# Kernel optimization log

Hardware: AMD Instinct MI355X
Metric: run time of the kernel (lower is better)

The kernel has to match this reference:

```python
import jax, jax.numpy as jnp
import numpy as np

C_PARAM = 2.0
EPS = 1e-05

def setup_inputs() -> dict:
    key = jax.random.key(0)
    x = jax.random.normal(key, (2048, 512, 7, 7), dtype=jnp.float32)
    return {"x": x}

def reference(x) -> jnp.ndarray:
    # y[n,c] = spatial mean over HW
    y = jnp.mean(x, axis=(2, 3))                      # [N, C]
    # per-sample channel stats (biased variance, matching mean(x^2)-mean^2)
    m = jnp.mean(y, axis=1, keepdims=True)            # [N, 1]
    mx2 = jnp.mean(y * y, axis=1, keepdims=True)      # [N, 1]
    var = jnp.maximum(mx2 - m * m, 0.0)
    inv_std = jax.lax.rsqrt(var + EPS)
    y_norm = (y - m) * inv_std                        # [N, C]
    gate = jnp.exp(-0.5 * C_PARAM * y_norm * y_norm)  # [N, C]
    return x * gate[:, :, None, None]
```

## Files before the change

kernel.cpp:

```cpp
#include <hip/hip_runtime.h>
#include <math.h>


#define NN 2048
#define CC 512
#define HW 49
#define CHCH 128
#define CHEL (CHCH * HW)
#define CHV4 (CHEL / 4)
#define NCHUNK (CC / CHCH)
#define EPS 1e-5f

__global__ __launch_bounds__(512) void stats_kernel(const float* __restrict__ x,
                                                    float* __restrict__ gate) {
    __shared__ float lds[CHEL];
    __shared__ float wsum[8];
    __shared__ float wsum2[8];
    __shared__ float s_m, s_inv;

    const int n = blockIdx.x;
    const int tid = threadIdx.x;
    const size_t nbase = (size_t)n * (CC * HW);
    const float4* __restrict__ xin4 = (const float4*)(x + nbase);

    float y = 0.0f;
    for (int j = 0; j < NCHUNK; ++j) {
        for (int i = tid; i < CHV4; i += 512) {
            ((float4*)lds)[i] = xin4[j * CHV4 + i];
        }
        __syncthreads();
        if ((tid >> 7) == j) {
            const int base = (tid & (CHCH - 1)) * HW;
            float s = 0.0f;
#pragma unroll
            for (int l = 0; l < HW; ++l) s += lds[base + l];
            y = s * (1.0f / (float)HW);
        }
        __syncthreads();
    }

    float sum = y, sum2 = y * y;
#pragma unroll
    for (int off = 32; off > 0; off >>= 1) {
        sum  += __shfl_down(sum, off);
        sum2 += __shfl_down(sum2, off);
    }
    const int wave = tid >> 6;
    const int lane = tid & 63;
    if (lane == 0) { wsum[wave] = sum; wsum2[wave] = sum2; }
    __syncthreads();
    if (tid == 0) {
        float ts = 0.0f, ts2 = 0.0f;
#pragma unroll
        for (int w = 0; w < 8; ++w) { ts += wsum[w]; ts2 += wsum2[w]; }
        const float m = ts * (1.0f / (float)CC);
        float var = ts2 * (1.0f / (float)CC) - m * m;
        var = fmaxf(var, 0.0f);
        s_m = m;
        s_inv = rsqrtf(var + EPS);
    }
    __syncthreads();

    const float yn = (y - s_m) * s_inv;
    gate[(size_t)n * CC + tid] = expf(-yn * yn);
}

__global__ __launch_bounds__(256) void apply_kernel(const float* __restrict__ x,
                                                    const float* __restrict__ gate,
                                                    float* __restrict__ out) {
    const unsigned i  = blockIdx.x * 256u + threadIdx.x;
    const unsigned e0 = i * 4u;
    const unsigned d0 = e0 / 49u;
    const unsigned r0 = e0 - d0 * 49u;

    const float4 v = ((const float4*)x)[i];
    const float g0 = gate[d0];
    const float g1 = (r0 >= 46u) ? gate[d0 + 1] : g0;

    float4 o;
    o.x = v.x * g0;
    o.y = v.y * ((r0 >= 48u) ? g1 : g0);
    o.z = v.z * ((r0 >= 47u) ? g1 : g0);
    o.w = v.w * ((r0 >= 46u) ? g1 : g0);
    ((float4*)out)[i] = o;
}

extern "C" void kernel_launch(void* const* d_in, const int* in_sizes, int n_in,
                              void* d_out, int out_size, void* d_ws, size_t ws_size,
                              hipStream_t stream) {
    const float* x = (const float*)d_in[0];
    float* out = (float*)d_out;
    float* gate = (float*)d_ws;

    stats_kernel<<<NN, 512, 0, stream>>>(x, gate);

    const int total4 = NN * CC * HW / 4;
    apply_kernel<<<total4 / 256, 256, 0, stream>>>(x, gate, out);
}
```

Measured before the change: 375.1 us.

## Fuse gate computation and apply pass into a single per-sample kernel

Merges the stats and apply kernels into one kernel where each block computes its sample's gate into shared memory and then scales that sample's slice of x. This removes the gate round-trip through global memory and one kernel launch. The second read of x (100KB per sample) now happens right after the first, so it may hit in L2/MALL cache rather than DRAM. The apply phase now runs with only 2048 blocks of 512 threads and carries the stats-phase LDS footprint, which may limit memory-level parallelism.

Result: faster. 359.5 us (-4.2%).

```diff
diff --git a/kernel.cpp b/kernel.cpp
--- a/kernel.cpp
+++ b/kernel.cpp
@@ -9,13 +9,14 @@
 #define CHEL (CHCH * HW)
 #define CHV4 (CHEL / 4)
 #define NCHUNK (CC / CHCH)
+#define SV4 (CC * HW / 4)
 #define EPS 1e-5f
 
-__global__ __launch_bounds__(512) void stats_kernel(const float* __restrict__ x,
-                                                    float* __restrict__ gate) {
+__global__ __launch_bounds__(512) void gate_kernel(const float* __restrict__ x,
+                                                   float* __restrict__ out) {
     __shared__ float lds[CHEL];
-    __shared__ float wsum[8];
-    __shared__ float wsum2[8];
+    __shared__ float gate_s[CC];
+    __shared__ float wsum[8], wsum2[8];
     __shared__ float s_m, s_inv;
 
     const int n = blockIdx.x;
@@ -25,9 +26,8 @@
 
     float y = 0.0f;
     for (int j = 0; j < NCHUNK; ++j) {
-        for (int i = tid; i < CHV4; i += 512) {
+        for (int i = tid; i < CHV4; i += 512)
             ((float4*)lds)[i] = xin4[j * CHV4 + i];
-        }
         __syncthreads();
         if ((tid >> 7) == j) {
             const int base = (tid & (CHCH - 1)) * HW;
@@ -45,44 +45,37 @@
         sum  += __shfl_down(sum, off);
         sum2 += __shfl_down(sum2, off);
     }
-    const int wave = tid >> 6;
-    const int lane = tid & 63;
-    if (lane == 0) { wsum[wave] = sum; wsum2[wave] = sum2; }
+    if ((tid & 63) == 0) { wsum[tid >> 6] = sum; wsum2[tid >> 6] = sum2; }
     __syncthreads();
     if (tid == 0) {
         float ts = 0.0f, ts2 = 0.0f;
 #pragma unroll
         for (int w = 0; w < 8; ++w) { ts += wsum[w]; ts2 += wsum2[w]; }
         const float m = ts * (1.0f / (float)CC);
-        float var = ts2 * (1.0f / (float)CC) - m * m;
-        var = fmaxf(var, 0.0f);
+        float var = fmaxf(ts2 * (1.0f / (float)CC) - m * m, 0.0f);
         s_m = m;
         s_inv = rsqrtf(var + EPS);
     }
     __syncthreads();
+    const float yn = (y - s_m) * s_inv;
+    gate_s[tid] = expf(-yn * yn);
+    __syncthreads();
 
-    const float yn = (y - s_m) * s_inv;
-    gate[(size_t)n * CC + tid] = expf(-yn * yn);
-}
-
-__global__ __launch_bounds__(256) void apply_kernel(const float* __restrict__ x,
-                                                    const float* __restrict__ gate,
-                                                    float* __restrict__ out) {
-    const unsigned i  = blockIdx.x * 256u + threadIdx.x;
-    const unsigned e0 = i * 4u;
-    const unsigned d0 = e0 / 49u;
-    const unsigned r0 = e0 - d0 * 49u;
-
-    const float4 v = ((const float4*)x)[i];
-    const float g0 = gate[d0];
-    const float g1 = (r0 >= 46u) ? gate[d0 + 1] : g0;
-
-    float4 o;
-    o.x = v.x * g0;
-    o.y = v.y * ((r0 >= 48u) ? g1 : g0);
-    o.z = v.z * ((r0 >= 47u) ? g1 : g0);
-    o.w = v.w * ((r0 >= 46u) ? g1 : g0);
-    ((float4*)out)[i] = o;
+    float4* __restrict__ out4 = (float4*)(out + nbase);
+    for (int i = tid; i < SV4; i += 512) {
+        const float4 v = xin4[i];
+        const unsigned e0 = 4u * (unsigned)i;
+        const unsigned d0 = e0 / 49u;
+        const unsigned r0 = e0 - d0 * 49u;
+        const float g0 = gate_s[d0];
+        const float g1 = (r0 >= 46u) ? gate_s[d0 + 1] : g0;
+        float4 o;
+        o.x = v.x * g0;
+        o.y = v.y * ((r0 >= 48u) ? g1 : g0);
+        o.z = v.z * ((r0 >= 47u) ? g1 : g0);
+        o.w = v.w * ((r0 >= 46u) ? g1 : g0);
+        out4[i] = o;
+    }
 }
 
 extern "C" void kernel_launch(void* const* d_in, const int* in_sizes, int n_in,
@@ -90,10 +83,5 @@
                               hipStream_t stream) {
     const float* x = (const float*)d_in[0];
     float* out = (float*)d_out;
-    float* gate = (float*)d_ws;
-
-    stats_kernel<<<NN, 512, 0, stream>>>(x, gate);
-
-    const int total4 = NN * CC * HW / 4;
-    apply_kernel<<<total4 / 256, 256, 0, stream>>>(x, gate, out);
+    gate_kernel<<<NN, 512, 0, stream>>>(x, out);
 }
```
